# Optimization experiments

Hardware: AMD Instinct MI355X
Metric: run time of the kernel (lower is better)

## Reference

```python
import jax, jax.numpy as jnp
import numpy as np

WS = 32      # window_size
P = 4        # patch size inside window
HEADS = 8
DIM_HEAD = 64
INNER = HEADS * DIM_HEAD  # 512
SCALE = DIM_HEAD ** -0.5


def setup_inputs() -> dict:
    key = jax.random.key(0)
    k1, k2, k3 = jax.random.split(key, 3)
    B, C, S = 8, 64, 256
    token_dim = P * P * C  # 1024
    x = jax.random.normal(k1, (B, C, S, S), dtype=jnp.float32)
    w_qkv = jax.random.normal(k2, (token_dim, 3 * INNER), dtype=jnp.float32) * (token_dim ** -0.5)
    w_out = jax.random.normal(k3, (INNER, token_dim), dtype=jnp.float32) * (INNER ** -0.5)
    b_out = jnp.zeros((token_dim,), dtype=jnp.float32)
    return {"x": x, "w_qkv": w_qkv, "w_out": w_out, "b_out": b_out}


def reference(x, w_qkv, w_out, b_out):
    B, C, H, W = x.shape
    H1, W1 = H // WS, W // WS
    # --- divide_regions: b c (h1 h) (w1 w) -> (b h1 w1) c h w ---
    xw = x.reshape(B, C, H1, WS, W1, WS).transpose(0, 2, 4, 1, 3, 5)
    xw = xw.reshape(B * H1 * W1, C, WS, WS)          # [n, C, ws, ws]
    n = xw.shape[0]
    nh = WS // P                                      # patches per side
    # patchify window: n c (nh p1) (nw p2) -> n (nh nw) (p1 p2 c)
    t = xw.reshape(n, C, nh, P, nh, P).transpose(0, 2, 4, 3, 5, 1)
    tokens = t.reshape(n, nh * nh, P * P * C)         # [n, T, D]
    # --- attention ---
    qkv = jnp.einsum('ntd,de->nte', tokens, w_qkv)    # [n, T, 3*inner]
    q, k, v = jnp.split(qkv, 3, axis=-1)
    def heads(a):
        return a.reshape(n, -1, HEADS, DIM_HEAD).transpose(0, 2, 1, 3)  # [n,h,T,dh]
    q, k, v = heads(q), heads(k), heads(v)
    attn = jax.nn.softmax(jnp.einsum('nhqd,nhkd->nhqk', q, k) * SCALE, axis=-1)
    o = jnp.einsum('nhqk,nhkd->nhqd', attn, v)        # [n,h,T,dh]
    o = o.transpose(0, 2, 1, 3).reshape(n, nh * nh, INNER)
    o = jnp.einsum('nte,ed->ntd', o, w_out) + b_out   # [n, T, D]
    # un-patchify: n (nh nw) (p1 p2 c) -> n c (nh p1) (nw p2)
    o = o.reshape(n, nh, nh, P, P, C).transpose(0, 5, 1, 3, 2, 4)
    o = o.reshape(n, C, WS, WS)
    # --- combine_regions: (b h1 w1) c h w -> b c (h1 h) (w1 w) ---
    o = o.reshape(B, H1, W1, C, WS, WS).transpose(0, 3, 1, 4, 2, 5)
    return o.reshape(B, C, H, W)
```

## Files before the change

### kernel.cpp

```cpp
#include <hip/hip_runtime.h>
#include <hip/hip_bf16.h>
#include <stdint.h>

typedef __attribute__((ext_vector_type(8))) short short8;
typedef __attribute__((ext_vector_type(4))) float floatx4;

constexpr int TD    = 1024;
constexpr int E3    = 1536;
constexpr int INNER = 512;
constexpr int NW    = 512;
constexpr int M_    = NW * 64;


constexpr size_t OFF_TOKA = 0;
constexpr size_t OFF_QKV  = (size_t)M_ * TD * 2;
constexpr size_t OFF_WQT  = OFF_QKV + (size_t)M_ * E3 * 2;
constexpr size_t OFF_WOT  = OFF_WQT + (size_t)E3 * TD * 2;
constexpr size_t OFF_BO   = OFF_WOT + (size_t)TD * INNER * 2;
constexpr size_t WS_NEED  = OFF_BO + TD * 4;

__device__ __forceinline__ void gl_lds16(const void* g, void* l) {
  __builtin_amdgcn_global_load_lds(
      (const __attribute__((address_space(1))) void*)g,
      (__attribute__((address_space(3))) void*)l, 16, 0, 0);
}

__global__ __launch_bounds__(256) void k_patchify(const float* __restrict__ x,
                                                  __hip_bfloat16* __restrict__ tokA) {
  __shared__ __hip_bfloat16 tok[8][1032];
  const int bid = blockIdx.x;
  const int n = bid >> 3, i = bid & 7;
  const int b = n >> 6, h1 = (n >> 3) & 7, w1 = n & 7;
  const int tid = threadIdx.x;
  for (int it = 0; it < 8; ++it) {
    int idx = it * 256 + tid;
    int w4 = idx & 7, p1 = (idx >> 3) & 3, c = idx >> 5;
    int h = h1 * 32 + i * 4 + p1;
    const float4 v = *(const float4*)&x[(((b * 64 + c) * 256 + h) * 256 + w1 * 32 + w4 * 4)];
    __hip_bfloat16* dst = &tok[w4][c * 16 + p1 * 4];
    dst[0] = __float2bfloat16(v.x);
    dst[1] = __float2bfloat16(v.y);
    dst[2] = __float2bfloat16(v.z);
    dst[3] = __float2bfloat16(v.w);
  }
  __syncthreads();
  for (int it = 0; it < 4; ++it) {
    int idx = it * 256 + tid;
    int ch = idx & 127, j = idx >> 7;
    uint4 v = *(const uint4*)&tok[j][ch * 8];
    *(uint4*)&tokA[(size_t)(n * 64 + i * 8 + j) * 1024 + ch * 8] = v;
  }
}

__global__ __launch_bounds__(256) void k_perm_wqkv(const float* __restrict__ wqkv,
                                                   __hip_bfloat16* __restrict__ wqT) {
  __shared__ __hip_bfloat16 wt[16][1032];
  const int e0 = blockIdx.x * 16, tid = threadIdx.x;
  for (int it = 0; it < 64; ++it) {
    int idx = it * 256 + tid;
    int e = idx & 15, d = idx >> 4;
    float v = wqkv[d * 1536 + e0 + e];
    int p1 = d >> 8, p2 = (d >> 6) & 3, c = d & 63;
    wt[e][c * 16 + p1 * 4 + p2] = __float2bfloat16(v);
  }
  __syncthreads();
  for (int it = 0; it < 8; ++it) {
    int idx = it * 256 + tid;
    int ch = idx & 127, e = idx >> 7;
    uint4 v = *(const uint4*)&wt[e][ch * 8];
    *(uint4*)&wqT[(size_t)(e0 + e) * 1024 + ch * 8] = v;
  }
}

__global__ __launch_bounds__(256) void k_perm_wout(const float* __restrict__ wout,
                                                   __hip_bfloat16* __restrict__ woT) {
  __shared__ __hip_bfloat16 wt[16][1032];
  const int e0 = blockIdx.x * 16, tid = threadIdx.x;
  for (int it = 0; it < 64; ++it) {
    int idx = it * 256 + tid;
    int d = idx & 1023, e = idx >> 10;
    float v = wout[(e0 + e) * 1024 + d];
    int p1 = d >> 8, p2 = (d >> 6) & 3, c = d & 63;
    wt[e][c * 16 + p1 * 4 + p2] = __float2bfloat16(v);
  }
  __syncthreads();
  for (int it = 0; it < 64; ++it) {
    int idx = it * 256 + tid;
    int e = idx & 15, dp = idx >> 4;
    woT[(size_t)dp * 512 + e0 + e] = wt[e][dp];
  }
}

__global__ __launch_bounds__(256) void k_perm_bias(const float* __restrict__ bout,
                                                   float* __restrict__ boP) {
  int dp = blockIdx.x * 256 + threadIdx.x;
  int c = dp >> 4, p1 = (dp >> 2) & 3, p2 = dp & 3;
  boP[dp] = bout[p1 * 256 + p2 * 64 + c];
}

template<int K>
__device__ __forceinline__ void gemm256_acc(
    const __hip_bfloat16* __restrict__ A,
    const __hip_bfloat16* __restrict__ Bt,
    int m0, int n0, int tid,
    __hip_bfloat16 (*As)[256][64], __hip_bfloat16 (*Bs)[256][64],
    floatx4 (&acc)[8][4])
{
  const int lane = tid & 63, wid = tid >> 6;
  const int wm = wid >> 2, wn = wid & 3;
  const int l15 = lane & 15, quad = lane >> 4;

  const int rl8 = tid >> 3;
  const int ch0 = (tid & 7) ^ (rl8 & 7);
  const __hip_bfloat16* Abase = A  + (size_t)(m0 + rl8) * K + ch0 * 8;
  const __hip_bfloat16* Bbase = Bt + (size_t)(n0 + rl8) * K + ch0 * 8;

  auto stageB = [&](int tile, int half, int buf) {
#pragma unroll
    for (int j = 0; j < 2; ++j)
      gl_lds16(Bbase + (size_t)(half * 128 + j * 64) * K + tile * 64,
               (char*)&Bs[buf][0][0] + half * 16384 + (j * 512 + tid) * 16);
  };
  auto stageA = [&](int tile, int chunk, int buf) {
#pragma unroll
    for (int j = 0; j < 2; ++j)
      gl_lds16(Abase + (size_t)(j * 128 + chunk * 64) * K + tile * 64,
               (char*)&As[buf][0][0] + j * 16384 + chunk * 8192 + tid * 16);
  };

  short8 af[2][2][2];
  short8 bf[4][2];

#define VM6 asm volatile("s_waitcnt vmcnt(6)" ::: "memory")
#define VM0 asm volatile("s_waitcnt vmcnt(0)" ::: "memory")

#define PH(CS, QC, BUFC, LDB, QN, BUFN, PFAF, STAGE, VMW)                         \
  do {                                                                            \
    if (LDB) {                                                                    \
      _Pragma("unroll") for (int n = 0; n < 4; ++n) {                             \
        const int rb = wn * 64 + n * 16 + l15;                                    \
        _Pragma("unroll") for (int kh = 0; kh < 2; ++kh)                          \
          bf[n][kh] = *(const short8*)&Bs[BUFC][rb][((kh * 4 + quad) ^ (rb & 7)) * 8]; \
      }                                                                           \
    }                                                                             \
    if (PFAF) {                                                                   \
      _Pragma("unroll") for (int m2 = 0; m2 < 2; ++m2) {                          \
        const int r = wm * 128 + (2 * (QN) + m2) * 16 + l15;                      \
        _Pragma("unroll") for (int kh = 0; kh < 2; ++kh)                          \
          af[(CS) ^ 1][m2][kh] = *(const short8*)&As[BUFN][r][((kh * 4 + quad) ^ (r & 7)) * 8]; \
      }                                                                           \
    }                                                                             \
    STAGE;                                                                        \
    __builtin_amdgcn_s_barrier();                                                 \
    __builtin_amdgcn_sched_barrier(0);                                            \
    __builtin_amdgcn_s_setprio(1);                                                \
    _Pragma("unroll") for (int kh = 0; kh < 2; ++kh)                              \
      _Pragma("unroll") for (int m2 = 0; m2 < 2; ++m2)                            \
        _Pragma("unroll") for (int n = 0; n < 4; ++n)                             \
          acc[2 * (QC) + m2][n] = __builtin_amdgcn_mfma_f32_16x16x32_bf16(        \
              af[CS][m2][kh], bf[n][kh], acc[2 * (QC) + m2][n], 0, 0, 0);         \
    __builtin_amdgcn_s_setprio(0);                                                \
    __builtin_amdgcn_sched_barrier(0);                                            \
    VMW;                                                                          \
    __builtin_amdgcn_s_barrier();                                                 \
    __builtin_amdgcn_sched_barrier(0);                                            \
  } while (0)

  stageB(0, 0, 0); stageB(0, 1, 0); stageA(0, 0, 0); stageA(0, 1, 0);
  stageB(1, 0, 1); stageB(1, 1, 1); stageA(1, 0, 1);
  VM6;
  __builtin_amdgcn_s_barrier();
  __builtin_amdgcn_sched_barrier(0);
#pragma unroll
  for (int m2 = 0; m2 < 2; ++m2) {
    const int r = wm * 128 + m2 * 16 + l15;
#pragma unroll
    for (int kh = 0; kh < 2; ++kh)
      af[0][m2][kh] = *(const short8*)&As[0][r][((kh * 4 + quad) ^ (r & 7)) * 8];
  }

  constexpr int NIT = K / 128;
#pragma unroll 1
  for (int i = 0; i < NIT - 1; ++i) {
    const int t1 = 2 * i + 1, t2 = 2 * i + 2, t3 = 2 * i + 3;
    PH(0, 0, 0, 1, 1, 0, 1, stageA(t1, 1, 1), VM6);
    PH(1, 1, 0, 0, 2, 0, 1, stageB(t2, 0, 0), );
    PH(0, 2, 0, 0, 3, 0, 1, stageB(t2, 1, 0), VM6);
    PH(1, 3, 0, 0, 0, 1, 1, stageA(t2, 0, 0), );
    PH(0, 0, 1, 1, 1, 1, 1, stageA(t2, 1, 0), VM6);
    PH(1, 1, 1, 0, 2, 1, 1, stageB(t3, 0, 1), );
    PH(0, 2, 1, 0, 3, 1, 1, stageB(t3, 1, 1), VM6);
    PH(1, 3, 1, 0, 0, 0, 1, stageA(t3, 0, 1), );
  }
  {
    const int tE = 2 * NIT - 1;
    PH(0, 0, 0, 1, 1, 0, 1, stageA(tE, 1, 1), VM6);
    PH(1, 1, 0, 0, 2, 0, 1, , );
    PH(0, 2, 0, 0, 3, 0, 1, , VM0);
    PH(1, 3, 0, 0, 0, 1, 1, , );
    PH(0, 0, 1, 1, 1, 1, 1, , );
    PH(1, 1, 1, 0, 2, 1, 1, , );
    PH(0, 2, 1, 0, 3, 1, 1, , );
    PH(1, 3, 1, 0, 0, 0, 0, , );
  }
#undef PH
#undef VM6
#undef VM0
}

__global__ __launch_bounds__(512, 2) void k_gemm_qkv(const __hip_bfloat16* __restrict__ A,
                                                     const __hip_bfloat16* __restrict__ Bt,
                                                     __hip_bfloat16* __restrict__ Cmat) {
  __shared__ __hip_bfloat16 As[2][256][64];
  __shared__ __hip_bfloat16 Bs[2][256][64];
  const int tid = threadIdx.x;
  const int bid = blockIdx.x;
  const int swz = (bid & 7) * 96 + (bid >> 3);
  const int n0 = (swz % 6) * 256, m0 = (swz / 6) * 256;
  floatx4 acc[8][4] = {};
  gemm256_acc<1024>(A, Bt, m0, n0, tid, As, Bs, acc);
  const int lane = tid & 63, wid = tid >> 6;
  const int wm = wid >> 2, wn = wid & 3;
  const int l15 = lane & 15, quad = lane >> 4;
#pragma unroll
  for (int mt = 0; mt < 8; ++mt)
#pragma unroll
    for (int nt = 0; nt < 4; ++nt) {
      const int col = n0 + wn * 64 + nt * 16 + l15;
#pragma unroll
      for (int r = 0; r < 4; ++r) {
        const int row = m0 + wm * 128 + mt * 16 + quad * 4 + r;
        Cmat[(size_t)row * 1536 + col] = __float2bfloat16(acc[mt][nt][r]);
      }
    }
}

__global__ __launch_bounds__(256) void k_attn(const __hip_bfloat16* __restrict__ qkv,
                                              __hip_bfloat16* __restrict__ oattn) {
  __shared__ __hip_bfloat16 Qs[64 * 64];
  __shared__ __hip_bfloat16 Ks[64 * 64];
  __shared__ __hip_bfloat16 Vt[64 * 72];
  __shared__ __hip_bfloat16 Ps[64 * 72];
  const int win = blockIdx.x, head = blockIdx.y;
  const int tid = threadIdx.x, lane = tid & 63, wid = tid >> 6;
  const int l15 = lane & 15, quad = lane >> 4;
  const int sx = l15 & 7;
  const size_t base = (size_t)win * 64 * 1536 + head * 64;
  for (int l = 0; l < 2; ++l) {
    int idx = l * 256 + tid;
    int t = idx >> 3, ch = idx & 7;
    const size_t rowb = base + (size_t)t * 1536 + ch * 8;
    uint4 q = *(const uint4*)&qkv[rowb];
    uint4 k = *(const uint4*)&qkv[rowb + 512];
    uint4 v = *(const uint4*)&qkv[rowb + 1024];
    const int pos = (ch ^ (t & 7)) * 8;
    *(uint4*)&Qs[t * 64 + pos] = q;
    *(uint4*)&Ks[t * 64 + pos] = k;
    *(uint4*)&Ps[t * 64 + pos] = v;
  }
  __syncthreads();
  {
    const int t = tid & 63, w = tid >> 6;
#pragma unroll
    for (int jn = 0; jn < 2; ++jn) {
      int j = w * 2 + jn;
      short8 v = *(const short8*)&Ps[t * 64 + ((j ^ (t & 7)) * 8)];
#pragma unroll
      for (int jj = 0; jj < 8; ++jj) Vt[(j * 8 + jj) * 72 + t] = ((__hip_bfloat16*)&v)[jj];
    }
  }
  __syncthreads();
  floatx4 sacc[4] = {};
#pragma unroll
  for (int kk = 0; kk < 64; kk += 32) {
    const int pos = (((kk >> 3) + quad) ^ sx) * 8;
    short8 aq = *(const short8*)&Qs[(wid * 16 + l15) * 64 + pos];
#pragma unroll
    for (int ct = 0; ct < 4; ++ct) {
      short8 bk = *(const short8*)&Ks[(ct * 16 + l15) * 64 + pos];
      sacc[ct] = __builtin_amdgcn_mfma_f32_16x16x32_bf16(aq, bk, sacc[ct], 0, 0, 0);
    }
  }
#pragma unroll
  for (int ct = 0; ct < 4; ++ct)
#pragma unroll
    for (int r = 0; r < 4; ++r) sacc[ct][r] = sacc[ct][r] * 0.125f;
#pragma unroll
  for (int r = 0; r < 4; ++r) {
    float m = fmaxf(fmaxf(sacc[0][r], sacc[1][r]), fmaxf(sacc[2][r], sacc[3][r]));
    m = fmaxf(m, __shfl_xor(m, 1));
    m = fmaxf(m, __shfl_xor(m, 2));
    m = fmaxf(m, __shfl_xor(m, 4));
    m = fmaxf(m, __shfl_xor(m, 8));
    float ev[4]; float s0 = 0.f;
#pragma unroll
    for (int ct = 0; ct < 4; ++ct) { ev[ct] = __expf(sacc[ct][r] - m); s0 += ev[ct]; }
    s0 += __shfl_xor(s0, 1);
    s0 += __shfl_xor(s0, 2);
    s0 += __shfl_xor(s0, 4);
    s0 += __shfl_xor(s0, 8);
    float inv = 1.0f / s0;
    int row = wid * 16 + quad * 4 + r;
#pragma unroll
    for (int ct = 0; ct < 4; ++ct)
      Ps[row * 72 + ct * 16 + l15] = __float2bfloat16(ev[ct] * inv);
  }
  __syncthreads();
  floatx4 oacc[4] = {};
#pragma unroll
  for (int kk = 0; kk < 64; kk += 32) {
    const int q8 = quad * 8;
    short8 ap = *(const short8*)&Ps[(wid * 16 + l15) * 72 + kk + q8];
#pragma unroll
    for (int nt = 0; nt < 4; ++nt) {
      short8 bv = *(const short8*)&Vt[(nt * 16 + l15) * 72 + kk + q8];
      oacc[nt] = __builtin_amdgcn_mfma_f32_16x16x32_bf16(ap, bv, oacc[nt], 0, 0, 0);
    }
  }
#pragma unroll
  for (int nt = 0; nt < 4; ++nt) {
    int dh = nt * 16 + l15;
#pragma unroll
    for (int r = 0; r < 4; ++r) {
      int t = wid * 16 + quad * 4 + r;
      oattn[((size_t)win * 64 + t) * 512 + head * 64 + dh] = __float2bfloat16(oacc[nt][r]);
    }
  }
}

__global__ __launch_bounds__(512, 2) void k_gemm_out(const __hip_bfloat16* __restrict__ A,
                                                     const __hip_bfloat16* __restrict__ Bt,
                                                     const float* __restrict__ bias,
                                                     float* __restrict__ out) {
  __shared__ __hip_bfloat16 As[2][256][64];
  __shared__ __hip_bfloat16 Bs[2][256][64];
  const int tid = threadIdx.x;
  const int bid = blockIdx.x;
  const int swz = (bid & 7) * 64 + (bid >> 3);
  const int n0 = (swz & 3) * 256, m0 = (swz >> 2) * 256;
  floatx4 acc[8][4] = {};
  gemm256_acc<512>(A, Bt, m0, n0, tid, As, Bs, acc);
  const int lane = tid & 63, wid = tid >> 6;
  const int wm = wid >> 2, wn = wid & 3;
  const int l15 = lane & 15, quad = lane >> 4;
#pragma unroll
  for (int nt = 0; nt < 4; ++nt) {
    const int dp = n0 + wn * 64 + nt * 16 + l15;
    const float bv = bias[dp];
    const int c = dp >> 4, p1 = (dp >> 2) & 3, p2 = dp & 3;
#pragma unroll
    for (int mt = 0; mt < 8; ++mt)
#pragma unroll
      for (int r = 0; r < 4; ++r) {
        const int m = m0 + wm * 128 + mt * 16 + quad * 4 + r;
        const int win = m >> 6, t = m & 63;
        const int i = t >> 3, j = t & 7;
        const int b = win >> 6, h1 = (win >> 3) & 7, w1 = win & 7;
        const int h = h1 * 32 + i * 4 + p1, w = w1 * 32 + j * 4 + p2;
        out[((b * 64 + c) * 256 + h) * 256 + w] = acc[mt][nt][r] + bv;
      }
  }
}

extern "C" void kernel_launch(void* const* d_in, const int* in_sizes, int n_in,
                              void* d_out, int out_size, void* d_ws, size_t ws_size,
                              hipStream_t stream) {
  const float* x    = (const float*)d_in[0];
  const float* wqkv = (const float*)d_in[1];
  const float* wout = (const float*)d_in[2];
  const float* bout = (const float*)d_in[3];
  float* out = (float*)d_out;
  char* ws = (char*)d_ws;
  if (ws_size < WS_NEED) return;

  __hip_bfloat16* tokA  = (__hip_bfloat16*)(ws + OFF_TOKA);
  __hip_bfloat16* oattn = (__hip_bfloat16*)(ws + OFF_TOKA);
  __hip_bfloat16* qkv   = (__hip_bfloat16*)(ws + OFF_QKV);
  __hip_bfloat16* wqT   = (__hip_bfloat16*)(ws + OFF_WQT);
  __hip_bfloat16* woT   = (__hip_bfloat16*)(ws + OFF_WOT);
  float* boP = (float*)(ws + OFF_BO);

  k_perm_wqkv<<<96, 256, 0, stream>>>(wqkv, wqT);
  k_perm_wout<<<32, 256, 0, stream>>>(wout, woT);
  k_perm_bias<<<4, 256, 0, stream>>>(bout, boP);
  k_patchify<<<4096, 256, 0, stream>>>(x, tokA);
  k_gemm_qkv<<<768, 512, 0, stream>>>(tokA, wqT, qkv);
  k_attn<<<dim3(512, 8), 256, 0, stream>>>(qkv, oattn);
  k_gemm_out<<<512, 512, 0, stream>>>(oattn, woT, boP, out);
}
```

Measured before the change: 444.7 us.

## Split QKV GEMM launch, add LDS waitcnts, and parallelize weight permutes

The QKV GEMM is now launched twice, once for the first 1024 output columns and once for the last 512, with a generalized block swizzle. This is meant to avoid a partial last wave of 768 blocks at two blocks per CU. The GEMM pipeline gains explicit lgkmcnt waits after the barrier and moves the scheduling barrier ahead of it, which tightens LDS read ordering. The weight permute kernels are split across more blocks with smaller LDS tiles to raise parallelism. The second launch adds launch overhead and a tail of its own.

Result: no change. 440.7 us (-0.9%).

```diff
diff --git a/kernel.cpp b/kernel.cpp
--- a/kernel.cpp
+++ b/kernel.cpp
@@ -54,40 +54,44 @@
 
 __global__ __launch_bounds__(256) void k_perm_wqkv(const float* __restrict__ wqkv,
                                                    __hip_bfloat16* __restrict__ wqT) {
-  __shared__ __hip_bfloat16 wt[16][1032];
-  const int e0 = blockIdx.x * 16, tid = threadIdx.x;
-  for (int it = 0; it < 64; ++it) {
-    int idx = it * 256 + tid;
-    int e = idx & 15, d = idx >> 4;
+  __shared__ __hip_bfloat16 wt[16][520];
+  const int e0 = blockIdx.x * 16, by = blockIdx.y, tid = threadIdx.x;
+  for (int it = 0; it < 32; ++it) {
+    int idx = it * 256 + tid;
+    int e = idx & 15, dl = idx >> 4;
+    int d = by * 512 + dl;
     float v = wqkv[d * 1536 + e0 + e];
-    int p1 = d >> 8, p2 = (d >> 6) & 3, c = d & 63;
-    wt[e][c * 16 + p1 * 4 + p2] = __float2bfloat16(v);
-  }
-  __syncthreads();
-  for (int it = 0; it < 8; ++it) {
-    int idx = it * 256 + tid;
-    int ch = idx & 127, e = idx >> 7;
+    int c = d & 63, off = (d >> 6) & 7;
+    wt[e][c * 8 + off] = __float2bfloat16(v);
+  }
+  __syncthreads();
+  for (int it = 0; it < 4; ++it) {
+    int idx = it * 256 + tid;
+    int ch = idx & 63, e = idx >> 6;
     uint4 v = *(const uint4*)&wt[e][ch * 8];
-    *(uint4*)&wqT[(size_t)(e0 + e) * 1024 + ch * 8] = v;
+    *(uint4*)&wqT[(size_t)(e0 + e) * 1024 + ch * 16 + by * 8] = v;
   }
 }
 
 __global__ __launch_bounds__(256) void k_perm_wout(const float* __restrict__ wout,
                                                    __hip_bfloat16* __restrict__ woT) {
-  __shared__ __hip_bfloat16 wt[16][1032];
-  const int e0 = blockIdx.x * 16, tid = threadIdx.x;
-  for (int it = 0; it < 64; ++it) {
-    int idx = it * 256 + tid;
-    int d = idx & 1023, e = idx >> 10;
+  __shared__ __hip_bfloat16 wt[4][520];
+  const int e0 = blockIdx.x * 4, by = blockIdx.y, tid = threadIdx.x;
+  for (int it = 0; it < 8; ++it) {
+    int idx = it * 256 + tid;
+    int dl = idx & 511, e = idx >> 9;
+    int d = by * 512 + dl;
     float v = wout[(e0 + e) * 1024 + d];
-    int p1 = d >> 8, p2 = (d >> 6) & 3, c = d & 63;
-    wt[e][c * 16 + p1 * 4 + p2] = __float2bfloat16(v);
-  }
-  __syncthreads();
-  for (int it = 0; it < 64; ++it) {
-    int idx = it * 256 + tid;
-    int e = idx & 15, dp = idx >> 4;
-    woT[(size_t)dp * 512 + e0 + e] = wt[e][dp];
+    int c = d & 63, off = (d >> 6) & 7;
+    wt[e][c * 8 + off] = __float2bfloat16(v);
+  }
+  __syncthreads();
+  for (int it = 0; it < 8; ++it) {
+    int idx = it * 256 + tid;
+    int e = idx & 3, sl = idx >> 2;
+    int c = sl >> 3, off = sl & 7;
+    int dp = c * 16 + by * 8 + off;
+    woT[(size_t)dp * 512 + e0 + e] = wt[e][sl];
   }
 }
 
@@ -133,17 +137,21 @@
 
 #define VM6 asm volatile("s_waitcnt vmcnt(6)" ::: "memory")
 #define VM0 asm volatile("s_waitcnt vmcnt(0)" ::: "memory")
-
-#define PH(CS, QC, BUFC, LDB, QN, BUFN, PFAF, STAGE, VMW)                         \
+#define LGKM4 do { asm volatile("s_waitcnt lgkmcnt(4)" ::: "memory"); \
+                   __builtin_amdgcn_sched_barrier(0); } while (0)
+#define LGKM0 do { asm volatile("s_waitcnt lgkmcnt(0)" ::: "memory"); \
+                   __builtin_amdgcn_sched_barrier(0); } while (0)
+
+#define PH(CS, QC, BUFC, LDB, QN, BUFN, PF, STAGE, VMW, LG)                       \
   do {                                                                            \
-    if (LDB) {                                                                    \
+    if (LDB) {                              \
       _Pragma("unroll") for (int n = 0; n < 4; ++n) {                             \
         const int rb = wn * 64 + n * 16 + l15;                                    \
         _Pragma("unroll") for (int kh = 0; kh < 2; ++kh)                          \
           bf[n][kh] = *(const short8*)&Bs[BUFC][rb][((kh * 4 + quad) ^ (rb & 7)) * 8]; \
       }                                                                           \
     }                                                                             \
-    if (PFAF) {                                                                   \
+    if (PF) {                                                                     \
       _Pragma("unroll") for (int m2 = 0; m2 < 2; ++m2) {                          \
         const int r = wm * 128 + (2 * (QN) + m2) * 16 + l15;                      \
         _Pragma("unroll") for (int kh = 0; kh < 2; ++kh)                          \
@@ -151,8 +159,9 @@
       }                                                                           \
     }                                                                             \
     STAGE;                                                                        \
+    __builtin_amdgcn_sched_barrier(0);                                            \
     __builtin_amdgcn_s_barrier();                                                 \
-    __builtin_amdgcn_sched_barrier(0);                                            \
+    LG;                                                                           \
     __builtin_amdgcn_s_setprio(1);                                                \
     _Pragma("unroll") for (int kh = 0; kh < 2; ++kh)                              \
       _Pragma("unroll") for (int m2 = 0; m2 < 2; ++m2)                            \
@@ -183,40 +192,45 @@
 #pragma unroll 1
   for (int i = 0; i < NIT - 1; ++i) {
     const int t1 = 2 * i + 1, t2 = 2 * i + 2, t3 = 2 * i + 3;
-    PH(0, 0, 0, 1, 1, 0, 1, stageA(t1, 1, 1), VM6);
-    PH(1, 1, 0, 0, 2, 0, 1, stageB(t2, 0, 0), );
-    PH(0, 2, 0, 0, 3, 0, 1, stageB(t2, 1, 0), VM6);
-    PH(1, 3, 0, 0, 0, 1, 1, stageA(t2, 0, 0), );
-    PH(0, 0, 1, 1, 1, 1, 1, stageA(t2, 1, 0), VM6);
-    PH(1, 1, 1, 0, 2, 1, 1, stageB(t3, 0, 1), );
-    PH(0, 2, 1, 0, 3, 1, 1, stageB(t3, 1, 1), VM6);
-    PH(1, 3, 1, 0, 0, 0, 1, stageA(t3, 0, 1), );
+    PH(0, 0, 0, 1, 1, 0, 1, stageA(t1, 1, 1), VM6, LGKM4);
+    PH(1, 1, 0, 0, 2, 0, 1, stageB(t2, 0, 0),    , LGKM4);
+    PH(0, 2, 0, 0, 3, 0, 1, stageB(t2, 1, 0), VM6, LGKM4);
+    PH(1, 3, 0, 0, 0, 1, 1, stageA(t2, 0, 0),    , LGKM4);
+    PH(0, 0, 1, 1, 1, 1, 1, stageA(t2, 1, 0), VM6, LGKM4);
+    PH(1, 1, 1, 0, 2, 1, 1, stageB(t3, 0, 1),    , LGKM4);
+    PH(0, 2, 1, 0, 3, 1, 1, stageB(t3, 1, 1), VM6, LGKM4);
+    PH(1, 3, 1, 0, 0, 0, 1, stageA(t3, 0, 1),    , LGKM4);
   }
   {
     const int tE = 2 * NIT - 1;
-    PH(0, 0, 0, 1, 1, 0, 1, stageA(tE, 1, 1), VM6);
-    PH(1, 1, 0, 0, 2, 0, 1, , );
-    PH(0, 2, 0, 0, 3, 0, 1, , VM0);
-    PH(1, 3, 0, 0, 0, 1, 1, , );
-    PH(0, 0, 1, 1, 1, 1, 1, , );
-    PH(1, 1, 1, 0, 2, 1, 1, , );
-    PH(0, 2, 1, 0, 3, 1, 1, , );
-    PH(1, 3, 1, 0, 0, 0, 0, , );
+    PH(0, 0, 0, 1, 1, 0, 1, stageA(tE, 1, 1), VM6, LGKM4);
+    PH(1, 1, 0, 0, 2, 0, 1, ,    , LGKM4);
+    PH(0, 2, 0, 0, 3, 0, 1, , VM0, LGKM4);
+    PH(1, 3, 0, 0, 0, 1, 1, ,    , LGKM4);
+    PH(0, 0, 1, 1, 1, 1, 1, ,    , LGKM4);
+    PH(1, 1, 1, 0, 2, 1, 1, ,    , LGKM4);
+    PH(0, 2, 1, 0, 3, 1, 1, ,    , LGKM4);
+    PH(1, 3, 1, 0, 0, 0, 0, ,    , LGKM0);
   }
 #undef PH
 #undef VM6
 #undef VM0
+#undef LGKM4
+#undef LGKM0
 }
 
 __global__ __launch_bounds__(512, 2) void k_gemm_qkv(const __hip_bfloat16* __restrict__ A,
                                                      const __hip_bfloat16* __restrict__ Bt,
-                                                     __hip_bfloat16* __restrict__ Cmat) {
+                                                     __hip_bfloat16* __restrict__ Cmat,
+                                                     int lognb, int nbase) {
   __shared__ __hip_bfloat16 As[2][256][64];
   __shared__ __hip_bfloat16 Bs[2][256][64];
   const int tid = threadIdx.x;
   const int bid = blockIdx.x;
-  const int swz = (bid & 7) * 96 + (bid >> 3);
-  const int n0 = (swz % 6) * 256, m0 = (swz / 6) * 256;
+  const int cpx = gridDim.x >> 3;
+  const int swz = (bid & 7) * cpx + (bid >> 3);
+  const int nb1 = (1 << lognb) - 1;
+  const int n0 = nbase + (swz & nb1) * 256, m0 = (swz >> lognb) * 256;
   floatx4 acc[8][4] = {};
   gemm256_acc<1024>(A, Bt, m0, n0, tid, As, Bs, acc);
   const int lane = tid & 63, wid = tid >> 6;
@@ -380,11 +394,12 @@
   __hip_bfloat16* woT   = (__hip_bfloat16*)(ws + OFF_WOT);
   float* boP = (float*)(ws + OFF_BO);
 
-  k_perm_wqkv<<<96, 256, 0, stream>>>(wqkv, wqT);
-  k_perm_wout<<<32, 256, 0, stream>>>(wout, woT);
+  k_perm_wqkv<<<dim3(96, 2), 256, 0, stream>>>(wqkv, wqT);
+  k_perm_wout<<<dim3(128, 2), 256, 0, stream>>>(wout, woT);
   k_perm_bias<<<4, 256, 0, stream>>>(bout, boP);
   k_patchify<<<4096, 256, 0, stream>>>(x, tokA);
-  k_gemm_qkv<<<768, 512, 0, stream>>>(tokA, wqT, qkv);
+  k_gemm_qkv<<<512, 512, 0, stream>>>(tokA, wqT, qkv, 2, 0);
+  k_gemm_qkv<<<256, 512, 0, stream>>>(tokA, wqT, qkv, 1, 1024);
   k_attn<<<dim3(512, 8), 256, 0, stream>>>(qkv, oattn);
   k_gemm_out<<<512, 512, 0, stream>>>(oattn, woT, boP, out);
 }
```
